# Performance work log

Measured on AMD Instinct MI355X. Metric: run time of the kernel, lower is better.

Reference implementation:

```python
import jax, jax.numpy as jnp
import numpy as np

N_ROIS, R, IH, IW = 128, 28, 800, 800


def setup_inputs() -> dict:
    key = jax.random.key(0)
    k1, k2, k3, k4, k5 = jax.random.split(key, 5)
    masks = jax.random.uniform(k1, (N_ROIS, 1, R, R), dtype=jnp.float32)
    # Valid xyxy boxes in image-pixel scale (to_img_scale output).
    cx = jax.random.uniform(k2, (N_ROIS, 1), minval=130.0, maxval=IW - 130.0)
    cy = jax.random.uniform(k3, (N_ROIS, 1), minval=130.0, maxval=IH - 130.0)
    w = jax.random.uniform(k4, (N_ROIS, 1), minval=40.0, maxval=260.0)
    h = jax.random.uniform(k5, (N_ROIS, 1), minval=40.0, maxval=260.0)
    boxes = jnp.concatenate([cx - w / 2, cy - h / 2, cx + w / 2, cy + h / 2], axis=1)
    return {"masks": masks, "boxes": boxes, "iH": IH, "iW": IW}


def _paste(masks, boxes, iH, iW):
    """mmdet _do_paste_mask with skip_empty=False: per-RoI affine grid +
    bilinear grid_sample (align_corners=False, zeros padding) into canvas.
    Grid is an outer product (x depends only on col, y only on row), so
    bilinear sampling is done separably: rows first, then columns."""
    N, _, rH, rW = masks.shape
    x0, y0, x1, y1 = (boxes[:, i:i + 1] for i in range(4))  # each [N,1]
    img_y = jnp.arange(iH, dtype=masks.dtype) + 0.5
    img_x = jnp.arange(iW, dtype=masks.dtype) + 0.5
    gy = (img_y[None, :] - y0) / (y1 - y0) * 2.0 - 1.0  # [N, iH] in [-1,1]
    gx = (img_x[None, :] - x0) / (x1 - x0) * 2.0 - 1.0  # [N, iW]
    # normalized -> input pixel coords (align_corners=False)
    py = (gy + 1.0) * (rH / 2.0) - 0.5
    px = (gx + 1.0) * (rW / 2.0) - 0.5
    yf = jnp.floor(py)
    xf = jnp.floor(px)
    wy = (py - yf)[:, None, :, None]  # [N,1,iH,1]
    wx = (px - xf)[:, None, None, :]  # [N,1,1,iW]
    y0i = yf.astype(jnp.int32)
    x0i = xf.astype(jnp.int32)

    def take_rows(iy):  # iy: [N, iH] -> [N,1,iH,rW], zeros outside
        valid = ((iy >= 0) & (iy < rH))[:, None, :, None]
        iyc = jnp.clip(iy, 0, rH - 1)
        rows = jnp.take_along_axis(masks, iyc[:, None, :, None], axis=2)
        return rows * valid

    ry = take_rows(y0i) * (1.0 - wy) + take_rows(y0i + 1) * wy  # [N,1,iH,rW]

    def take_cols(ix):  # ix: [N, iW] -> [N,1,iH,iW], zeros outside
        valid = ((ix >= 0) & (ix < rW))[:, None, None, :]
        ixc = jnp.clip(ix, 0, rW - 1)
        cols = jnp.take_along_axis(ry, ixc[:, None, None, :], axis=3)
        return cols * valid

    out = take_cols(x0i) * (1.0 - wx) + take_cols(x0i + 1) * wx
    return out[:, 0]  # [N, iH, iW]


def reference(masks, boxes, iH, iW):
    return _paste(masks, boxes, iH, iW)
```

## Files before the change

### kernel.cpp

```cpp
#include <hip/hip_runtime.h>


#define RR 28
#define IMG 800
#define PX_PER_THREAD 4
#define ROW_THREADS (IMG / PX_PER_THREAD)

__global__ __launch_bounds__(256) void roi_paste_kernel(
    const float* __restrict__ masks,
    const float* __restrict__ boxes,
    float* __restrict__ out) {
  const int y = blockIdx.x;
  const int n = blockIdx.y;

  const float x0 = boxes[n * 4 + 0];
  const float y0 = boxes[n * 4 + 1];
  const float x1 = boxes[n * 4 + 2];
  const float y1 = boxes[n * 4 + 3];

  __shared__ float ry[RR];
  const float py = ((float)y + 0.5f - y0) / (y1 - y0) * (float)RR - 0.5f;
  const float yfl = floorf(py);
  const float wy = py - yfl;
  const int yi = (int)yfl;

  const int t = threadIdx.x;
  if (t < RR) {
    const float* mrow = masks + (size_t)n * RR * RR;
    float a = (yi >= 0 && yi < RR)          ? mrow[yi * RR + t]       : 0.0f;
    float b = (yi + 1 >= 0 && yi + 1 < RR)  ? mrow[(yi + 1) * RR + t] : 0.0f;
    ry[t] = a * (1.0f - wy) + b * wy;
  }
  __syncthreads();

  if (t < ROW_THREADS) {
    const float xscale = (float)RR / (x1 - x0);
    const int xb = t * PX_PER_THREAD;
    float v[PX_PER_THREAD];
#pragma unroll
    for (int k = 0; k < PX_PER_THREAD; ++k) {
      const float px = ((float)(xb + k) + 0.5f - x0) * xscale - 0.5f;
      const float xfl = floorf(px);
      const float wx = px - xfl;
      const int xi = (int)xfl;
      const float a = (xi >= 0 && xi < RR)         ? ry[xi]     : 0.0f;
      const float b = (xi + 1 >= 0 && xi + 1 < RR) ? ry[xi + 1] : 0.0f;
      v[k] = a * (1.0f - wx) + b * wx;
    }
    float4 pack = make_float4(v[0], v[1], v[2], v[3]);
    *reinterpret_cast<float4*>(
        &out[((size_t)n * IMG + y) * IMG + xb]) = pack;
  }
}

extern "C" void kernel_launch(void* const* d_in, const int* in_sizes, int n_in,
                              void* d_out, int out_size, void* d_ws, size_t ws_size,
                              hipStream_t stream) {
  const float* masks = (const float*)d_in[0];
  const float* boxes = (const float*)d_in[1];
  float* out = (float*)d_out;

  dim3 grid(IMG, 128 );
  dim3 block(256);
  roi_paste_kernel<<<grid, block, 0, stream>>>(masks, boxes, out);
}
```

Measured before the change: 63.93 us.

## Process 16 rows per block with 128 threads and a flattened float4 loop

Each block now handles 16 output rows of one RoI instead of a single row. It precomputes all 16 row-interpolated mask rows in shared memory, then loops over the flattened float4 outputs with all 128 threads. This removes the 56 of 256 threads that sat idle per block, spreads per-block setup and sync over more output, and cuts the grid size. It also replaces branchy edge checks with clamped indices and zeroed weights. The kernel is a write-bound 327MB output, so gains depend on whether the old version already saturated store bandwidth.

```diff
diff --git a/kernel.cpp b/kernel.cpp
--- a/kernel.cpp
+++ b/kernel.cpp
@@ -3,53 +3,79 @@
 
 #define RR 28
 #define IMG 800
-#define PX_PER_THREAD 4
-#define ROW_THREADS (IMG / PX_PER_THREAD)
+#define ROWS_PER_BLOCK 16
+#define BLOCK 128
+#define F4_PER_ROW (IMG / 4)
+#define F4_PER_BLOCK (ROWS_PER_BLOCK * F4_PER_ROW)
+#define ITERS (F4_PER_BLOCK / BLOCK)
+#define GROUPS_PER_ROI (IMG / ROWS_PER_BLOCK)
 
-__global__ __launch_bounds__(256) void roi_paste_kernel(
+__global__ __launch_bounds__(BLOCK) void roi_paste_kernel(
     const float* __restrict__ masks,
     const float* __restrict__ boxes,
     float* __restrict__ out) {
-  const int y = blockIdx.x;
-  const int n = blockIdx.y;
+  const int bid = blockIdx.x;
+  const int n  = bid / GROUPS_PER_ROI;
+  const int rg = bid % GROUPS_PER_ROI;
+  const int rowbase = rg * ROWS_PER_BLOCK;
 
-  const float x0 = boxes[n * 4 + 0];
-  const float y0 = boxes[n * 4 + 1];
-  const float x1 = boxes[n * 4 + 2];
-  const float y1 = boxes[n * 4 + 3];
+  const float bx0 = boxes[n * 4 + 0];
+  const float by0 = boxes[n * 4 + 1];
+  const float bx1 = boxes[n * 4 + 2];
+  const float by1 = boxes[n * 4 + 3];
+  const float sx = (float)RR / (bx1 - bx0);
+  const float cx = (0.5f - bx0) * sx - 0.5f;
+  const float sy = (float)RR / (by1 - by0);
+  const float cy = (0.5f - by0) * sy - 0.5f;
 
-  __shared__ float ry[RR];
-  const float py = ((float)y + 0.5f - y0) / (y1 - y0) * (float)RR - 0.5f;
-  const float yfl = floorf(py);
-  const float wy = py - yfl;
-  const int yi = (int)yfl;
+  __shared__ float ry[ROWS_PER_BLOCK * RR];
 
-  const int t = threadIdx.x;
-  if (t < RR) {
-    const float* mrow = masks + (size_t)n * RR * RR;
-    float a = (yi >= 0 && yi < RR)          ? mrow[yi * RR + t]       : 0.0f;
-    float b = (yi + 1 >= 0 && yi + 1 < RR)  ? mrow[(yi + 1) * RR + t] : 0.0f;
-    ry[t] = a * (1.0f - wy) + b * wy;
+  const float* mbase = masks + (size_t)n * (RR * RR);
+  for (int e = threadIdx.x; e < ROWS_PER_BLOCK * RR; e += BLOCK) {
+    const int r = e / RR;
+    const int c = e - r * RR;
+    const float py = fmaf((float)(rowbase + r), sy, cy);
+    const float yf = floorf(py);
+    const float wy = py - yf;
+    const int yi = (int)yf;
+    const bool va = (unsigned)yi < (unsigned)RR;
+    const bool vb = (unsigned)(yi + 1) < (unsigned)RR;
+    const int ya = min(max(yi, 0), RR - 1);
+    const int yb = min(max(yi + 1, 0), RR - 1);
+    const float a = va ? mbase[ya * RR + c] : 0.0f;
+    const float b = vb ? mbase[yb * RR + c] : 0.0f;
+    ry[e] = a * (1.0f - wy) + b * wy;
   }
   __syncthreads();
 
-  if (t < ROW_THREADS) {
-    const float xscale = (float)RR / (x1 - x0);
-    const int xb = t * PX_PER_THREAD;
-    float v[PX_PER_THREAD];
+  float* oblock = out + ((size_t)n * IMG + rowbase) * IMG;
+
+#pragma unroll 1
+  for (int j = 0; j < ITERS; ++j) {
+    const unsigned i = (unsigned)(j * BLOCK) + threadIdx.x;
+    const unsigned row  = i / (unsigned)F4_PER_ROW;
+    const unsigned col4 = i - row * (unsigned)F4_PER_ROW;
+    const float* ryrow = ry + row * RR;
+    const float xbf = (float)(col4 * 4u);
+    float v[4];
 #pragma unroll
-    for (int k = 0; k < PX_PER_THREAD; ++k) {
-      const float px = ((float)(xb + k) + 0.5f - x0) * xscale - 0.5f;
-      const float xfl = floorf(px);
-      const float wx = px - xfl;
-      const int xi = (int)xfl;
-      const float a = (xi >= 0 && xi < RR)         ? ry[xi]     : 0.0f;
-      const float b = (xi + 1 >= 0 && xi + 1 < RR) ? ry[xi + 1] : 0.0f;
-      v[k] = a * (1.0f - wx) + b * wx;
+    for (int k = 0; k < 4; ++k) {
+      const float px = fmaf(xbf + (float)k, sx, cx);
+      const float xf = floorf(px);
+      const float wx = px - xf;
+      const int xi = (int)xf;
+      const bool va = (unsigned)xi < (unsigned)RR;
+      const bool vb = (unsigned)(xi + 1) < (unsigned)RR;
+      const int xa = min(max(xi, 0), RR - 1);
+      const int xb = min(max(xi + 1, 0), RR - 1);
+      const float a = ryrow[xa];
+      const float b = ryrow[xb];
+      const float wa = va ? (1.0f - wx) : 0.0f;
+      const float wb = vb ? wx : 0.0f;
+      v[k] = wa * a + wb * b;
     }
-    float4 pack = make_float4(v[0], v[1], v[2], v[3]);
-    *reinterpret_cast<float4*>(
-        &out[((size_t)n * IMG + y) * IMG + xb]) = pack;
+    *reinterpret_cast<float4*>(oblock + (size_t)row * IMG + col4 * 4u) =
+        make_float4(v[0], v[1], v[2], v[3]);
   }
 }
 
@@ -60,7 +86,8 @@
   const float* boxes = (const float*)d_in[1];
   float* out = (float*)d_out;
 
-  dim3 grid(IMG, 128 );
-  dim3 block(256);
+  const int n_rois = in_sizes[1] / 4;
+  dim3 grid(n_rois * GROUPS_PER_ROI);
+  dim3 block(BLOCK);
   roi_paste_kernel<<<grid, block, 0, stream>>>(masks, boxes, out);
 }
```

After: 64.86 us. No clear change (+1.5%).
